# Kernel optimization log

Hardware: AMD Instinct MI355X
Metric: run time of the kernel (lower is better)

Reference implementation:

```python
import jax, jax.numpy as jnp
import numpy as np

B, C, H, W = 2, 1024, 64, 64
R, E, HE, T, K = 16, 4, 512, 3, 2


def setup_inputs() -> dict:
    key = jax.random.key(0)
    ks = jax.random.split(key, 12)
    s = 0.02
    return {
        "x": jax.random.normal(ks[0], (B, C, H, W), jnp.float32),
        "t": jax.random.normal(ks[1], (B, C, H, W), jnp.float32),
        "fc_w": jax.random.normal(ks[2], (C, 2 * C), jnp.float32) * s,
        "ln_g": jnp.ones((C,), jnp.float32),
        "ln_b": jnp.zeros((C,), jnp.float32),
        "f1_w1": jax.random.normal(ks[3], (C // R, C), jnp.float32) * s,
        "f1_b1": jnp.zeros((C // R,), jnp.float32),
        "f1_wa": jax.random.normal(ks[4], (C, C // R), jnp.float32) * s,
        "f1_ba": jnp.zeros((C,), jnp.float32),
        "f1_wb": jax.random.normal(ks[5], (C, C // R), jnp.float32) * s,
        "f1_bb": jnp.zeros((C,), jnp.float32),
        "w_gate": jax.random.normal(ks[6], (T, C, E), jnp.float32) * s,
        "e_w1": jax.random.normal(ks[7], (E, C, HE), jnp.float32) * s,
        "e_b1": jnp.zeros((E, HE), jnp.float32),
        "e_w2": jax.random.normal(ks[8], (E, HE, C), jnp.float32) * s,
        "e_b2": jnp.zeros((E, C), jnp.float32),
        "task_index": 1,
    }


def _cv_squared(v):
    eps = 1e-10
    return jnp.var(v, ddof=1) / (jnp.mean(v) ** 2 + eps)


def reference(x, t, fc_w, ln_g, ln_b, f1_w1, f1_b1, f1_wa, f1_ba, f1_wb, f1_bb,
              w_gate, e_w1, e_b1, e_w2, e_b2, task_index):
    b, c, h, w = x.shape
    n = h * w
    # MultiTaskGeneralFusion: SE-style dual-branch channel gating
    s = jnp.mean(x + t, axis=(2, 3))                        # [B, C]
    hid = jax.nn.relu(s @ f1_w1.T + f1_b1)                  # [B, C/r]
    a = hid @ f1_wa.T + f1_ba                               # [B, C]
    bb = hid @ f1_wb.T + f1_bb                              # [B, C]
    wts = jax.nn.softmax(jnp.stack([a, bb], axis=0), axis=0)  # [2, B, C]
    z = wts[0][:, :, None, None] * x + wts[1][:, :, None, None] * t
    # fused linear -> ReLU -> LayerNorm on concatenated tokens
    x3 = x.reshape(b, c, n).transpose(0, 2, 1)              # [B, N, C]
    t3 = t.reshape(b, c, n).transpose(0, 2, 1)
    y = jnp.concatenate([x3, t3], axis=-1)                  # [B, N, 2C]
    y = jax.nn.relu(jnp.einsum('bnd,cd->bnc', y, fc_w))     # [B, N, C]
    mu = jnp.mean(y, axis=-1, keepdims=True)
    var = jnp.mean((y - mu) ** 2, axis=-1, keepdims=True)
    y = (y - mu) * jax.lax.rsqrt(var + 1e-5) * ln_g + ln_b
    yf = y.reshape(b * n, c)                                # [BN, C]
    # MMoE top-k gating (eval mode: no gating noise)
    logits = yf @ w_gate[task_index]                        # [BN, E]
    top_logits, top_idx = jax.lax.top_k(logits, K)          # [BN, K]
    top_gates = jax.nn.softmax(top_logits, axis=-1)
    gates = jnp.zeros_like(logits).at[jnp.arange(b * n)[:, None], top_idx].set(top_gates)
    # dense expert compute, gated combine
    eh = jax.nn.relu(jnp.einsum('nc,ech->neh', yf, e_w1) + e_b1)   # [BN, E, HE]
    eo = jnp.einsum('neh,eho->neo', eh, e_w2) + e_b2               # [BN, E, C]
    ym = jnp.einsum('ne,neo->no', gates, eo)                        # [BN, C]
    importance = gates.sum(axis=0)
    load = (gates > 0).sum(axis=0).astype(jnp.float32)
    aux_loss = _cv_squared(importance) + _cv_squared(load)
    y4 = ym.reshape(b, n, c).transpose(0, 2, 1).reshape(b, c, h, w) + z
    return (y4, aux_loss)
```

## Files before the change

kernel.cpp:

```cpp
#include <hip/hip_runtime.h>
#include <cstddef>
#include <cstdint>

#define B_   2
#define C_   1024
#define N_   4096
#define M_   8192
#define K2_  2048
#define E_   4
#define HE_  512

typedef float f32x4 __attribute__((ext_vector_type(4)));
typedef short bf16x8 __attribute__((ext_vector_type(8)));
typedef _Float16 f16x8 __attribute__((ext_vector_type(8)));
typedef unsigned short u16x8 __attribute__((ext_vector_type(8)));

#define WAITV(N) asm volatile("s_waitcnt vmcnt(" #N ")" ::: "memory")
#define WAITL0   asm volatile("s_waitcnt lgkmcnt(0)" ::: "memory")
#define SBAR     __builtin_amdgcn_sched_barrier(0)

static __device__ __forceinline__ unsigned short f2bf(float f) {
  unsigned int u = __float_as_uint(f);
  u = u + 0x7fffu + ((u >> 16) & 1u);
  return (unsigned short)(u >> 16);
}

static __device__ __forceinline__ void gl_lds16(const void* g, void* l) {
  __builtin_amdgcn_global_load_lds(
      (const __attribute__((address_space(1))) void*)(uintptr_t)g,
      (__attribute__((address_space(3))) void*)(unsigned)(uintptr_t)l,
      16, 0, 0);
}

__global__ __launch_bounds__(256) void k_se_gate(const float* __restrict__ s,
                                                 const float* __restrict__ w1, const float* __restrict__ b1,
                                                 const float* __restrict__ wa, const float* __restrict__ ba,
                                                 const float* __restrict__ wb, const float* __restrict__ bbv,
                                                 float* __restrict__ wts0) {
  __shared__ float hid[2][64];
  const int t = threadIdx.x;
  if (t < 128) {
    const int b = t >> 6, r = t & 63;
    float acc = b1[r];
    const float* sp = s + b * C_;
    const float* wp = w1 + r * C_;
    for (int c = 0; c < C_; ++c) acc = fmaf(sp[c], wp[c], acc);
    hid[b][r] = fmaxf(acc, 0.f);
  }
  __syncthreads();
  for (int o = t; o < B_ * C_; o += 256) {
    const int b = o >> 10, c = o & 1023;
    float a = ba[c], bb = bbv[c];
    #pragma unroll 8
    for (int r = 0; r < 64; ++r) {
      const float h = hid[b][r];
      a  = fmaf(h, wa[c * 64 + r], a);
      bb = fmaf(h, wb[c * 64 + r], bb);
    }
    wts0[o] = 1.f / (1.f + expf(bb - a));
  }
}

__global__ __launch_bounds__(256) void k_prep_act(const float* __restrict__ x,
                                                  const float* __restrict__ t,
                                                  _Float16* __restrict__ ah,
                                                  _Float16* __restrict__ am,
                                                  float* __restrict__ spart) {
  __shared__ float tile[64][65];
  const int c0 = blockIdx.x * 64, n0 = blockIdx.y * 64, b = blockIdx.z;
  const float* xb = x + (size_t)b * (C_ * N_);
  const float* tb = t + (size_t)b * (C_ * N_);
  _Float16* ahb = ah + (size_t)b * (N_ * (size_t)K2_);
  _Float16* amb = am + (size_t)b * (N_ * (size_t)K2_);
  const int tid = threadIdx.x;
  const int prow = tid >> 2, pseg = tid & 3;
  float psum = 0.f;
  #pragma unroll
  for (int srcsel = 0; srcsel < 2; ++srcsel) {
    const float* src = srcsel ? tb : xb;
    const int koff = srcsel ? C_ : 0;
    if (srcsel) __syncthreads();
    #pragma unroll
    for (int p = 0; p < 4; ++p) {
      const int f = tid + p * 256;
      const int cr = f >> 4, nq = f & 15;
      const float4 v = *(const float4*)(src + (size_t)(c0 + cr) * N_ + n0 + nq * 4);
      tile[cr][nq * 4 + 0] = v.x; tile[cr][nq * 4 + 1] = v.y;
      tile[cr][nq * 4 + 2] = v.z; tile[cr][nq * 4 + 3] = v.w;
    }
    __syncthreads();
    {
      float a = 0.f;
      #pragma unroll
      for (int u = 0; u < 16; ++u) a += tile[prow][pseg * 16 + u];
      psum += a;
    }
    #pragma unroll
    for (int p = 0; p < 2; ++p) {
      const int f = tid + p * 256;
      const int mr = f >> 3, kq = f & 7;
      f16x8 hv, mv;
      #pragma unroll
      for (int u = 0; u < 8; ++u) {
        const float v = tile[kq * 8 + u][mr] * 64.f;
        const _Float16 h = (_Float16)v;
        hv[u] = h;
        mv[u] = (_Float16)(v - (float)h);
      }
      const size_t off = (size_t)(n0 + mr) * K2_ + koff + c0 + kq * 8;
      *(f16x8*)(ahb + off) = hv;
      *(f16x8*)(amb + off) = mv;
    }
  }
  psum += __shfl_xor(psum, 1);
  psum += __shfl_xor(psum, 2);
  if (pseg == 0)
    spart[((size_t)(b * C_ + c0 + prow)) * 64 + blockIdx.y] = psum;
}

__global__ __launch_bounds__(256) void k_reduce2(const float* __restrict__ spart,
                                                 float* __restrict__ s) {
  const int idx = blockIdx.x * 256 + threadIdx.x;
  const float* p = spart + (size_t)idx * 64;
  float acc = 0.f;
  #pragma unroll
  for (int j = 0; j < 64; ++j) acc += p[j];
  s[idx] = acc * (1.f / (float)N_);
}

__global__ __launch_bounds__(256) void k_prep_fcw(const float* __restrict__ w,
                                                  _Float16* __restrict__ wh,
                                                  _Float16* __restrict__ wm) {
  const size_t i = ((size_t)blockIdx.x * 256 + threadIdx.x) * 8;
  const float4 v0 = *(const float4*)(w + i);
  const float4 v1 = *(const float4*)(w + i + 4);
  const float vv[8] = {v0.x, v0.y, v0.z, v0.w, v1.x, v1.y, v1.z, v1.w};
  f16x8 hv, mv;
  #pragma unroll
  for (int u = 0; u < 8; ++u) {
    const float sv = vv[u] * 4096.f;
    const _Float16 h = (_Float16)sv;
    hv[u] = h;
    mv[u] = (_Float16)(sv - (float)h);
  }
  *(f16x8*)(wh + i) = hv;
  *(f16x8*)(wm + i) = mv;
}

__global__ __launch_bounds__(256) void k_prep_tr(const float* __restrict__ src, long long zs, int srs,
                                                 unsigned short* __restrict__ dst, long long zo, int drs) {
  __shared__ float tile[64][65];
  const int c0 = blockIdx.x * 64, r0 = blockIdx.y * 64, z = blockIdx.z;
  const float* s = src + (size_t)z * zs;
  unsigned short* d = dst + (size_t)z * zo;
  const int tid = threadIdx.x;
  #pragma unroll
  for (int p = 0; p < 4; ++p) {
    const int f = tid + p * 256;
    const int rr = f >> 4, cq = f & 15;
    const float4 v = *(const float4*)(s + (size_t)(r0 + rr) * srs + c0 + cq * 4);
    tile[rr][cq * 4 + 0] = v.x; tile[rr][cq * 4 + 1] = v.y;
    tile[rr][cq * 4 + 2] = v.z; tile[rr][cq * 4 + 3] = v.w;
  }
  __syncthreads();
  #pragma unroll
  for (int p = 0; p < 2; ++p) {
    const int f = tid + p * 256;
    const int cr = f >> 3, rq = f & 7;
    u16x8 o;
    #pragma unroll
    for (int u = 0; u < 8; ++u) o[u] = f2bf(tile[rq * 8 + u][cr]);
    *(u16x8*)(d + (size_t)(c0 + cr) * drs + r0 + rq * 8) = o;
  }
}

__global__ __launch_bounds__(256) void k_fc_mfma(const _Float16* __restrict__ Ah,
                                                 const _Float16* __restrict__ Am,
                                                 const _Float16* __restrict__ Bh,
                                                 const _Float16* __restrict__ Bm,
                                                 float* __restrict__ y) {
  __shared__ __align__(16) char lds[2][32768];
  const int tid = threadIdx.x, w = tid >> 6, l = tid & 63;
  const int flat = blockIdx.x + blockIdx.y * 8;
  const int swz = (flat & 7) * 64 + (flat >> 3);
  const int n0 = (swz & 7) * 128, m0 = (swz >> 3) * 128;
  const int wr = w >> 1, wc = w & 1, lg = l >> 4, lr = l & 15;
  f32x4 acc[4][4] = {};
  const int sg = tid >> 7, sr = tid & 127;
  const size_t ga0 = (size_t)(m0 + sr) * K2_ + sg * 8;
  const size_t gb0 = (size_t)(n0 + sr) * K2_ + sg * 8;

  auto STAGE = [&](int buf, int k0) {
    char* b = &lds[buf][0] + w * 1024;
    gl_lds16(Ah + ga0 + k0, b);
    gl_lds16(Ah + ga0 + 16 + k0, b + 4096);
    gl_lds16(Am + ga0 + k0, b + 8192);
    gl_lds16(Am + ga0 + 16 + k0, b + 12288);
    gl_lds16(Bh + gb0 + k0, b + 16384);
    gl_lds16(Bh + gb0 + 16 + k0, b + 20480);
    gl_lds16(Bm + gb0 + k0, b + 24576);
    gl_lds16(Bm + gb0 + 16 + k0, b + 28672);
  };

  STAGE(0, 0);
  STAGE(1, 32);
  for (int it = 0; it < 64; ++it) {
    const int cur = it & 1;
    if (it < 63) { WAITV(8); } else { WAITV(0); }
    SBAR;
    __builtin_amdgcn_s_barrier();
    const char* bb = &lds[cur][0];
    f16x8 a_h[4], a_m[4], b_h[4], b_m[4];
    #pragma unroll
    for (int i = 0; i < 4; ++i) {
      const int off = lg * 2048 + (wr * 64 + i * 16 + lr) * 16;
      a_h[i] = *(const f16x8*)(bb + off);
      a_m[i] = *(const f16x8*)(bb + 8192 + off);
    }
    #pragma unroll
    for (int j = 0; j < 4; ++j) {
      const int off = lg * 2048 + (wc * 64 + j * 16 + lr) * 16;
      b_h[j] = *(const f16x8*)(bb + 16384 + off);
      b_m[j] = *(const f16x8*)(bb + 24576 + off);
    }
    #pragma unroll
    for (int i = 0; i < 4; ++i)
      #pragma unroll
      for (int j = 0; j < 4; ++j)
        acc[i][j] = __builtin_amdgcn_mfma_f32_16x16x32_f16(a_h[i], b_h[j], acc[i][j], 0, 0, 0);
    #pragma unroll
    for (int i = 0; i < 4; ++i)
      #pragma unroll
      for (int j = 0; j < 4; ++j)
        acc[i][j] = __builtin_amdgcn_mfma_f32_16x16x32_f16(a_h[i], b_m[j], acc[i][j], 0, 0, 0);
    #pragma unroll
    for (int i = 0; i < 4; ++i)
      #pragma unroll
      for (int j = 0; j < 4; ++j)
        acc[i][j] = __builtin_amdgcn_mfma_f32_16x16x32_f16(a_m[i], b_h[j], acc[i][j], 0, 0, 0);
    WAITL0;
    SBAR;
    __builtin_amdgcn_s_barrier();
    if (it < 62) STAGE(cur, (it + 2) * 32);
  }
  #pragma unroll
  for (int i = 0; i < 4; ++i) {
    const int mb = m0 + wr * 64 + i * 16 + lg * 4;
    #pragma unroll
    for (int j = 0; j < 4; ++j) {
      const int n = n0 + wc * 64 + j * 16 + lr;
      #pragma unroll
      for (int r = 0; r < 4; ++r)
        y[(size_t)(mb + r) * C_ + n] = fmaxf(acc[i][j][r] * (1.f / 262144.f), 0.f);
    }
  }
}

__global__ __launch_bounds__(256) void k_ln_topk(const float* __restrict__ y,
                                                 const float* __restrict__ lng, const float* __restrict__ lnb,
                                                 const float* __restrict__ wg, const int* __restrict__ taskp,
                                                 unsigned short* __restrict__ yf, float* __restrict__ gates) {
  const int wv = threadIdx.x >> 6, ln = threadIdx.x & 63;
  const int m = blockIdx.x * 4 + wv;
  const float* yr = y + (size_t)m * C_;
  float4 v[4];
  #pragma unroll
  for (int ch = 0; ch < 4; ++ch) v[ch] = *(const float4*)(yr + ch * 256 + ln * 4);
  float sum = 0.f;
  #pragma unroll
  for (int ch = 0; ch < 4; ++ch) sum += (v[ch].x + v[ch].y) + (v[ch].z + v[ch].w);
  #pragma unroll
  for (int o = 32; o; o >>= 1) sum += __shfl_down(sum, o);
  sum = __shfl(sum, 0);
  const float mu = sum * (1.f / 1024.f);
  float q = 0.f;
  #pragma unroll
  for (int ch = 0; ch < 4; ++ch) {
    const float dx = v[ch].x - mu, dy = v[ch].y - mu, dz = v[ch].z - mu, dw = v[ch].w - mu;
    q += (dx * dx + dy * dy) + (dz * dz + dw * dw);
  }
  #pragma unroll
  for (int o = 32; o; o >>= 1) q += __shfl_down(q, o);
  q = __shfl(q, 0);
  const float rstd = rsqrtf(q * (1.f / 1024.f) + 1e-5f);
  const float* wrow = wg + (size_t)(*taskp) * (C_ * E_);
  float l0 = 0.f, l1 = 0.f, l2 = 0.f, l3 = 0.f;
  #pragma unroll
  for (int ch = 0; ch < 4; ++ch) {
    const int c = ch * 256 + ln * 4;
    const float4 gg = *(const float4*)(lng + c);
    const float4 bv = *(const float4*)(lnb + c);
    float f[4];
    f[0] = (v[ch].x - mu) * rstd * gg.x + bv.x;
    f[1] = (v[ch].y - mu) * rstd * gg.y + bv.y;
    f[2] = (v[ch].z - mu) * rstd * gg.z + bv.z;
    f[3] = (v[ch].w - mu) * rstd * gg.w + bv.w;
    uint2 pk;
    pk.x = (unsigned)f2bf(f[0]) | ((unsigned)f2bf(f[1]) << 16);
    pk.y = (unsigned)f2bf(f[2]) | ((unsigned)f2bf(f[3]) << 16);
    *(uint2*)(yf + (size_t)m * C_ + c) = pk;
    #pragma unroll
    for (int i = 0; i < 4; ++i) {
      const float4 we = *(const float4*)(wrow + (size_t)(c + i) * 4);
      l0 = fmaf(f[i], we.x, l0); l1 = fmaf(f[i], we.y, l1);
      l2 = fmaf(f[i], we.z, l2); l3 = fmaf(f[i], we.w, l3);
    }
  }
  #pragma unroll
  for (int o = 32; o; o >>= 1) {
    l0 += __shfl_down(l0, o); l1 += __shfl_down(l1, o);
    l2 += __shfl_down(l2, o); l3 += __shfl_down(l3, o);
  }
  if (ln == 0) {
    const float L[4] = {l0, l1, l2, l3};
    int i1 = 0; float best = L[0];
    #pragma unroll
    for (int e = 1; e < 4; ++e) if (L[e] > best) { best = L[e]; i1 = e; }
    int i2 = -1; float s2 = 0.f;
    #pragma unroll
    for (int e = 0; e < 4; ++e) if (e != i1 && (i2 < 0 || L[e] > s2)) { s2 = L[e]; i2 = e; }
    const float g1 = 1.f / (1.f + expf(s2 - best));
    const float g2 = 1.f - g1;
    float4 gv;
    gv.x = (i1 == 0) ? g1 : ((i2 == 0) ? g2 : 0.f);
    gv.y = (i1 == 1) ? g1 : ((i2 == 1) ? g2 : 0.f);
    gv.z = (i1 == 2) ? g1 : ((i2 == 2) ? g2 : 0.f);
    gv.w = (i1 == 3) ? g1 : ((i2 == 3) ? g2 : 0.f);
    *(float4*)(gates + (size_t)m * 4) = gv;
  }
}

__global__ __launch_bounds__(256) void k_moe1_mfma(const unsigned short* __restrict__ yf,
                                                   const short* __restrict__ Bw,
                                                   const float* __restrict__ b1,
                                                   const float* __restrict__ gates,
                                                   unsigned short* __restrict__ ehg) {
  __shared__ __align__(16) char lds[2][16384];
  const int tid = threadIdx.x, w = tid >> 6, l = tid & 63;
  const int flat = blockIdx.x + blockIdx.y * 16;
  const int swz = (flat & 7) * 128 + (flat >> 3);
  const int n0 = (swz & 15) * 128, m0 = (swz >> 4) * 128;
  const int wr = w >> 1, wc = w & 1, lg = l >> 4, lr = l & 15;
  f32x4 acc[4][4] = {};
  const int sg = tid >> 7, sr = tid & 127;
  const size_t ga0 = (size_t)(m0 + sr) * C_ + sg * 8;
  const size_t gb0 = (size_t)(n0 + sr) * C_ + sg * 8;

  auto STAGE = [&](int buf, int k0) {
    char* b = &lds[buf][0] + w * 1024;
    gl_lds16(yf + ga0 + k0, b);
    gl_lds16(yf + ga0 + 16 + k0, b + 4096);
    gl_lds16(Bw + gb0 + k0, b + 8192);
    gl_lds16(Bw + gb0 + 16 + k0, b + 12288);
  };

  STAGE(0, 0);
  STAGE(1, 32);
  for (int it = 0; it < 32; ++it) {
    const int cur = it & 1;
    if (it < 31) { WAITV(4); } else { WAITV(0); }
    SBAR;
    __builtin_amdgcn_s_barrier();
    const char* bb = &lds[cur][0];
    bf16x8 af[4], bfr[4];
    #pragma unroll
    for (int i = 0; i < 4; ++i)
      af[i] = *(const bf16x8*)(bb + lg * 2048 + (wr * 64 + i * 16 + lr) * 16);
    #pragma unroll
    for (int j = 0; j < 4; ++j)
      bfr[j] = *(const bf16x8*)(bb + 8192 + lg * 2048 + (wc * 64 + j * 16 + lr) * 16);
    SBAR;
    __builtin_amdgcn_s_setprio(1);
    #pragma unroll
    for (int i = 0; i < 4; ++i)
      #pragma unroll
      for (int j = 0; j < 4; ++j)
        acc[i][j] = __builtin_amdgcn_mfma_f32_16x16x32_bf16(af[i], bfr[j], acc[i][j], 0, 0, 0);
    __builtin_amdgcn_s_setprio(0);
    WAITL0;
    SBAR;
    __builtin_amdgcn_s_barrier();
    if (it < 30) STAGE(cur, (it + 2) * 32);
  }
  const int e0 = n0 >> 9;
  #pragma unroll
  for (int j = 0; j < 4; ++j) {
    const int n = n0 + wc * 64 + j * 16 + lr;
    const float bias = b1[e0 * HE_ + (n & 511)];
    #pragma unroll
    for (int i = 0; i < 4; ++i) {
      const int mb = m0 + wr * 64 + i * 16 + lg * 4;
      #pragma unroll
      for (int r = 0; r < 4; ++r) {
        const float g = gates[(size_t)(mb + r) * 4 + e0];
        const float v = fmaxf(acc[i][j][r] + bias, 0.f) * g;
        ehg[(size_t)(mb + r) * K2_ + n] = f2bf(v);
      }
    }
  }
}

__global__ __launch_bounds__(256) void k_moe2_mfma(const short* __restrict__ Aeh,
                                                   const short* __restrict__ Bw,
                                                   const float* __restrict__ b2,
                                                   const float* __restrict__ gates,
                                                   float* __restrict__ ym) {
  __shared__ __align__(16) char lds[2][16384];
  const int tid = threadIdx.x, w = tid >> 6, l = tid & 63;
  const int flat = blockIdx.x + blockIdx.y * 8;
  const int swz = (flat & 7) * 64 + (flat >> 3);
  const int n0 = (swz & 7) * 128, m0 = (swz >> 3) * 128;
  const int wr = w >> 1, wc = w & 1, lg = l >> 4, lr = l & 15;
  f32x4 acc[4][4] = {};
  const int sg = tid >> 7, sr = tid & 127;
  const size_t ga0 = (size_t)(m0 + sr) * K2_ + sg * 8;
  const size_t gb0 = (size_t)(n0 + sr) * K2_ + sg * 8;

  auto STAGE = [&](int buf, int k0) {
    char* b = &lds[buf][0] + w * 1024;
    gl_lds16(Aeh + ga0 + k0, b);
    gl_lds16(Aeh + ga0 + 16 + k0, b + 4096);
    gl_lds16(Bw + gb0 + k0, b + 8192);
    gl_lds16(Bw + gb0 + 16 + k0, b + 12288);
  };

  STAGE(0, 0);
  STAGE(1, 32);
  for (int it = 0; it < 64; ++it) {
    const int cur = it & 1;
    if (it < 63) { WAITV(4); } else { WAITV(0); }
    SBAR;
    __builtin_amdgcn_s_barrier();
    const char* bb = &lds[cur][0];
    bf16x8 af[4], bfr[4];
    #pragma unroll
    for (int i = 0; i < 4; ++i)
      af[i] = *(const bf16x8*)(bb + lg * 2048 + (wr * 64 + i * 16 + lr) * 16);
    #pragma unroll
    for (int j = 0; j < 4; ++j)
      bfr[j] = *(const bf16x8*)(bb + 8192 + lg * 2048 + (wc * 64 + j * 16 + lr) * 16);
    SBAR;
    __builtin_amdgcn_s_setprio(1);
    #pragma unroll
    for (int i = 0; i < 4; ++i)
      #pragma unroll
      for (int j = 0; j < 4; ++j)
        acc[i][j] = __builtin_amdgcn_mfma_f32_16x16x32_bf16(af[i], bfr[j], acc[i][j], 0, 0, 0);
    __builtin_amdgcn_s_setprio(0);
    WAITL0;
    SBAR;
    __builtin_amdgcn_s_barrier();
    if (it < 62) STAGE(cur, (it + 2) * 32);
  }
  float bb2[4][4];
  #pragma unroll
  for (int j = 0; j < 4; ++j) {
    const int n = n0 + wc * 64 + j * 16 + lr;
    #pragma unroll
    for (int e = 0; e < 4; ++e) bb2[j][e] = b2[e * C_ + n];
  }
  #pragma unroll
  for (int i = 0; i < 4; ++i) {
    const int mb = m0 + wr * 64 + i * 16 + lg * 4;
    #pragma unroll
    for (int r = 0; r < 4; ++r) {
      const float4 g = *(const float4*)(gates + (size_t)(mb + r) * 4);
      #pragma unroll
      for (int j = 0; j < 4; ++j) {
        const int n = n0 + wc * 64 + j * 16 + lr;
        ym[(size_t)(mb + r) * C_ + n] =
            acc[i][j][r] + g.x * bb2[j][0] + g.y * bb2[j][1] + g.z * bb2[j][2] + g.w * bb2[j][3];
      }
    }
  }
}

__global__ __launch_bounds__(256) void k_aux(const float* __restrict__ gates, float* __restrict__ outp) {
  const int t = threadIdx.x;
  float imp[4] = {0, 0, 0, 0}, ld[4] = {0, 0, 0, 0};
  for (int m = t; m < M_; m += 256) {
    const float4 g = *(const float4*)(gates + (size_t)m * 4);
    imp[0] += g.x; imp[1] += g.y; imp[2] += g.z; imp[3] += g.w;
    ld[0] += (g.x > 0.f) ? 1.f : 0.f; ld[1] += (g.y > 0.f) ? 1.f : 0.f;
    ld[2] += (g.z > 0.f) ? 1.f : 0.f; ld[3] += (g.w > 0.f) ? 1.f : 0.f;
  }
  __shared__ float red[8][4];
  const int wv = t >> 6, ln = t & 63;
  #pragma unroll
  for (int e = 0; e < 4; ++e) {
    float a = imp[e], b = ld[e];
    #pragma unroll
    for (int o = 32; o; o >>= 1) { a += __shfl_down(a, o); b += __shfl_down(b, o); }
    if (ln == 0) { red[e][wv] = a; red[4 + e][wv] = b; }
  }
  __syncthreads();
  if (t == 0) {
    float I[4], L[4];
    #pragma unroll
    for (int e = 0; e < 4; ++e) {
      I[e] = red[e][0] + red[e][1] + red[e][2] + red[e][3];
      L[e] = red[4 + e][0] + red[4 + e][1] + red[4 + e][2] + red[4 + e][3];
    }
    const float mi = (I[0] + I[1] + I[2] + I[3]) * 0.25f;
    const float vi = ((I[0] - mi) * (I[0] - mi) + (I[1] - mi) * (I[1] - mi) +
                      (I[2] - mi) * (I[2] - mi) + (I[3] - mi) * (I[3] - mi)) / 3.f;
    const float ml = (L[0] + L[1] + L[2] + L[3]) * 0.25f;
    const float vl = ((L[0] - ml) * (L[0] - ml) + (L[1] - ml) * (L[1] - ml) +
                      (L[2] - ml) * (L[2] - ml) + (L[3] - ml) * (L[3] - ml)) / 3.f;
    *outp = vi / (mi * mi + 1e-10f) + vl / (ml * ml + 1e-10f);
  }
}

__global__ __launch_bounds__(256) void k_final(const float* __restrict__ ym,
                                               const float* __restrict__ x, const float* __restrict__ t,
                                               const float* __restrict__ wts0, float* __restrict__ out) {
  __shared__ float tile[64][65];
  const int c0 = blockIdx.x * 64, n0 = blockIdx.y * 64, b = blockIdx.z;
  const int tid = threadIdx.x;
  #pragma unroll
  for (int p = 0; p < 4; ++p) {
    const int f = tid + p * 256;
    const int row = f >> 4, cq = f & 15;
    const float4 v = *(const float4*)(ym + (size_t)(b * N_ + n0 + row) * C_ + c0 + cq * 4);
    tile[row][cq * 4 + 0] = v.x; tile[row][cq * 4 + 1] = v.y;
    tile[row][cq * 4 + 2] = v.z; tile[row][cq * 4 + 3] = v.w;
  }
  __syncthreads();
  #pragma unroll
  for (int p = 0; p < 4; ++p) {
    const int f = tid + p * 256;
    const int cr = f >> 4, nq = f & 15;
    const int c = c0 + cr;
    const float w0 = wts0[b * C_ + c];
    const float w1 = 1.f - w0;
    const size_t idx = (size_t)(b * C_ + c) * N_ + n0 + nq * 4;
    const float4 xv = *(const float4*)(x + idx);
    const float4 tv = *(const float4*)(t + idx);
    float4 o;
    o.x = tile[nq * 4 + 0][cr] + w0 * xv.x + w1 * tv.x;
    o.y = tile[nq * 4 + 1][cr] + w0 * xv.y + w1 * tv.y;
    o.z = tile[nq * 4 + 2][cr] + w0 * xv.z + w1 * tv.z;
    o.w = tile[nq * 4 + 3][cr] + w0 * xv.w + w1 * tv.w;
    *(float4*)(out + idx) = o;
  }
}

extern "C" void kernel_launch(void* const* d_in, const int* in_sizes, int n_in,
                              void* d_out, int out_size, void* d_ws, size_t ws_size,
                              hipStream_t stream) {
  const float* x     = (const float*)d_in[0];
  const float* t     = (const float*)d_in[1];
  const float* fc_w  = (const float*)d_in[2];
  const float* ln_g  = (const float*)d_in[3];
  const float* ln_b  = (const float*)d_in[4];
  const float* f1_w1 = (const float*)d_in[5];
  const float* f1_b1 = (const float*)d_in[6];
  const float* f1_wa = (const float*)d_in[7];
  const float* f1_ba = (const float*)d_in[8];
  const float* f1_wb = (const float*)d_in[9];
  const float* f1_bb = (const float*)d_in[10];
  const float* w_gate = (const float*)d_in[11];
  const float* e_w1  = (const float*)d_in[12];
  const float* e_b1  = (const float*)d_in[13];
  const float* e_w2  = (const float*)d_in[14];
  const float* e_b2  = (const float*)d_in[15];
  const int*   task  = (const int*)d_in[16];
  float* out = (float*)d_out;

  char* ws = (char*)d_ws;
  float*          y     = (float*)ws;
  float*          spart = (float*)ws;
  _Float16*       ah    = (_Float16*)(ws + 33554432);
  _Float16*       am    = (_Float16*)(ws + 67108864);
  unsigned short* yf    = (unsigned short*)(ws + 33554432);
  unsigned short* ehg   = (unsigned short*)(ws + 50331648);
  _Float16* wh  = (_Float16*)(ws + 100663296);
  _Float16* wm  = (_Float16*)(ws + 104857600);
  short*    w1t = (short*)(ws + 109051904);
  short*    w2t = (short*)(ws + 113246208);
  float* sbuf  = (float*)(ws + 117440512);
  float* wts0  = (float*)(ws + 117448704);
  float* gates = (float*)(ws + 117456896);

  k_prep_fcw<<<1024, 256, 0, stream>>>(fc_w, wh, wm);
  k_prep_tr<<<dim3(8, 16, 4), 256, 0, stream>>>(e_w1, 524288LL, 512, (unsigned short*)w1t, 524288LL, 1024);
  k_prep_tr<<<dim3(16, 8, 4), 256, 0, stream>>>(e_w2, 524288LL, 1024, (unsigned short*)w2t, 512LL, 2048);
  k_prep_act<<<dim3(16, 64, 2), 256, 0, stream>>>(x, t, ah, am, spart);
  k_reduce2<<<8, 256, 0, stream>>>(spart, sbuf);
  k_se_gate<<<1, 256, 0, stream>>>(sbuf, f1_w1, f1_b1, f1_wa, f1_ba, f1_wb, f1_bb, wts0);
  k_fc_mfma<<<dim3(8, 64), 256, 0, stream>>>(ah, am, wh, wm, y);
  k_ln_topk<<<M_ / 4, 256, 0, stream>>>(y, ln_g, ln_b, w_gate, task, yf, gates);
  k_moe1_mfma<<<dim3(16, 64), 256, 0, stream>>>(yf, w1t, e_b1, gates, ehg);
  k_moe2_mfma<<<dim3(8, 64), 256, 0, stream>>>((const short*)ehg, w2t, e_b2, gates, y);
  k_aux<<<1, 256, 0, stream>>>(gates, out + (size_t)B_ * C_ * N_);
  k_final<<<dim3(C_ / 64, N_ / 64, B_), 256, 0, stream>>>(y, x, t, wts0, out);
}
```

Measured before the change: 416.6 us.

## Enlarge FC GEMM tile to 256x128 with 512 threads and phased prefetch

The fused-linear GEMM kernel moves from 256-thread 128x128 tiles to 512-thread 256x128 tiles, so each B tile is reused across more rows. The global-to-LDS prefetch of the next K slice is split into three phases, each placed between the three MFMA groups (hi*hi, hi*lo, lo*hi), with partial vmcnt waits and s_setprio raised around MFMA bursts. The aim is to overlap loads with compute and halve B traffic. In exchange it uses more LDS (96KB per block), more barriers per iteration, and launches half as many blocks.

```diff
diff --git a/kernel.cpp b/kernel.cpp
--- a/kernel.cpp
+++ b/kernel.cpp
@@ -174,74 +174,125 @@
   }
 }
 
-__global__ __launch_bounds__(256) void k_fc_mfma(const _Float16* __restrict__ Ah,
-                                                 const _Float16* __restrict__ Am,
-                                                 const _Float16* __restrict__ Bh,
-                                                 const _Float16* __restrict__ Bm,
-                                                 float* __restrict__ y) {
-  __shared__ __align__(16) char lds[2][32768];
+__global__ __launch_bounds__(512, 2) void k_fc_mfma(const _Float16* __restrict__ Ah,
+                                                    const _Float16* __restrict__ Am,
+                                                    const _Float16* __restrict__ Bh,
+                                                    const _Float16* __restrict__ Bm,
+                                                    float* __restrict__ y) {
+  __shared__ __align__(16) char lds[2][49152];
   const int tid = threadIdx.x, w = tid >> 6, l = tid & 63;
   const int flat = blockIdx.x + blockIdx.y * 8;
-  const int swz = (flat & 7) * 64 + (flat >> 3);
-  const int n0 = (swz & 7) * 128, m0 = (swz >> 3) * 128;
+  const int swz = (flat & 7) * 32 + (flat >> 3);
+  const int n0 = (swz & 7) * 128, m0 = (swz >> 3) * 256;
   const int wr = w >> 1, wc = w & 1, lg = l >> 4, lr = l & 15;
   f32x4 acc[4][4] = {};
-  const int sg = tid >> 7, sr = tid & 127;
-  const size_t ga0 = (size_t)(m0 + sr) * K2_ + sg * 8;
-  const size_t gb0 = (size_t)(n0 + sr) * K2_ + sg * 8;
-
-  auto STAGE = [&](int buf, int k0) {
-    char* b = &lds[buf][0] + w * 1024;
-    gl_lds16(Ah + ga0 + k0, b);
-    gl_lds16(Ah + ga0 + 16 + k0, b + 4096);
-    gl_lds16(Am + ga0 + k0, b + 8192);
-    gl_lds16(Am + ga0 + 16 + k0, b + 12288);
-    gl_lds16(Bh + gb0 + k0, b + 16384);
-    gl_lds16(Bh + gb0 + 16 + k0, b + 20480);
-    gl_lds16(Bm + gb0 + k0, b + 24576);
-    gl_lds16(Bm + gb0 + 16 + k0, b + 28672);
+
+  auto LDA = [&](char* bufb, const _Float16* src, int roff, int k0, int q) {
+    const int chunk = q * 512 + tid;
+    const int kg = chunk >> 8, row = chunk & 255;
+    gl_lds16(src + (size_t)(m0 + row) * K2_ + k0 + kg * 8,
+             bufb + roff + (q * 512 + w * 64) * 16);
   };
-
-  STAGE(0, 0);
-  STAGE(1, 32);
-  for (int it = 0; it < 64; ++it) {
-    const int cur = it & 1;
-    if (it < 63) { WAITV(8); } else { WAITV(0); }
-    SBAR;
-    __builtin_amdgcn_s_barrier();
+  auto LDB = [&](char* bufb, const _Float16* src, int roff, int k0) {
+    const int kg = tid >> 7, row = tid & 127;
+    gl_lds16(src + (size_t)(n0 + row) * K2_ + k0 + kg * 8,
+             bufb + roff + (w * 64) * 16);
+  };
+
+  LDA(&lds[0][0], Ah, 0, 0, 0);
+  LDA(&lds[0][0], Ah, 0, 0, 1);
+  LDB(&lds[0][0], Bh, 32768, 0);
+  LDB(&lds[0][0], Bm, 40960, 0);
+  LDA(&lds[0][0], Am, 16384, 0, 0);
+  LDA(&lds[0][0], Am, 16384, 0, 1);
+
+  f16x8 a_h[4], b_h[4], b_m[4], a_m[4];
+  for (int t = 0; t < 63; ++t) {
+    const int cur = t & 1;
     const char* bb = &lds[cur][0];
-    f16x8 a_h[4], a_m[4], b_h[4], b_m[4];
-    #pragma unroll
-    for (int i = 0; i < 4; ++i) {
-      const int off = lg * 2048 + (wr * 64 + i * 16 + lr) * 16;
-      a_h[i] = *(const f16x8*)(bb + off);
-      a_m[i] = *(const f16x8*)(bb + 8192 + off);
-    }
-    #pragma unroll
-    for (int j = 0; j < 4; ++j) {
-      const int off = lg * 2048 + (wc * 64 + j * 16 + lr) * 16;
-      b_h[j] = *(const f16x8*)(bb + 16384 + off);
-      b_m[j] = *(const f16x8*)(bb + 24576 + off);
-    }
+    char* nb = &lds[cur ^ 1][0];
+    const int nk = (t + 1) * 32;
+    WAITV(3); SBAR;
+    __builtin_amdgcn_s_barrier();
+    LDA(nb, Ah, 0, nk, 0);
+    LDA(nb, Ah, 0, nk, 1);
+    #pragma unroll
+    for (int i = 0; i < 4; ++i)
+      a_h[i] = *(const f16x8*)(bb + (lg * 256 + wr * 64 + i * 16 + lr) * 16);
+    #pragma unroll
+    for (int j = 0; j < 4; ++j)
+      b_h[j] = *(const f16x8*)(bb + 32768 + (lg * 128 + wc * 64 + j * 16 + lr) * 16);
+    __builtin_amdgcn_s_setprio(1);
     #pragma unroll
     for (int i = 0; i < 4; ++i)
       #pragma unroll
       for (int j = 0; j < 4; ++j)
         acc[i][j] = __builtin_amdgcn_mfma_f32_16x16x32_f16(a_h[i], b_h[j], acc[i][j], 0, 0, 0);
+    __builtin_amdgcn_s_setprio(0);
+    WAITV(4); SBAR;
+    __builtin_amdgcn_s_barrier();
+    LDB(nb, Bh, 32768, nk);
+    LDB(nb, Bm, 40960, nk);
+    #pragma unroll
+    for (int j = 0; j < 4; ++j)
+      b_m[j] = *(const f16x8*)(bb + 40960 + (lg * 128 + wc * 64 + j * 16 + lr) * 16);
+    __builtin_amdgcn_s_setprio(1);
     #pragma unroll
     for (int i = 0; i < 4; ++i)
       #pragma unroll
       for (int j = 0; j < 4; ++j)
         acc[i][j] = __builtin_amdgcn_mfma_f32_16x16x32_f16(a_h[i], b_m[j], acc[i][j], 0, 0, 0);
+    __builtin_amdgcn_s_setprio(0);
+    WAITV(4); SBAR;
+    __builtin_amdgcn_s_barrier();
+    LDA(nb, Am, 16384, nk, 0);
+    LDA(nb, Am, 16384, nk, 1);
+    #pragma unroll
+    for (int i = 0; i < 4; ++i)
+      a_m[i] = *(const f16x8*)(bb + 16384 + (lg * 256 + wr * 64 + i * 16 + lr) * 16);
+    __builtin_amdgcn_s_setprio(1);
     #pragma unroll
     for (int i = 0; i < 4; ++i)
       #pragma unroll
       for (int j = 0; j < 4; ++j)
         acc[i][j] = __builtin_amdgcn_mfma_f32_16x16x32_f16(a_m[i], b_h[j], acc[i][j], 0, 0, 0);
-    WAITL0;
-    SBAR;
-    __builtin_amdgcn_s_barrier();
-    if (it < 62) STAGE(cur, (it + 2) * 32);
+    __builtin_amdgcn_s_setprio(0);
+  }
+  {
+    const char* bb = &lds[1][0];
+    WAITV(3); SBAR;
+    __builtin_amdgcn_s_barrier();
+    #pragma unroll
+    for (int i = 0; i < 4; ++i)
+      a_h[i] = *(const f16x8*)(bb + (lg * 256 + wr * 64 + i * 16 + lr) * 16);
+    #pragma unroll
+    for (int j = 0; j < 4; ++j)
+      b_h[j] = *(const f16x8*)(bb + 32768 + (lg * 128 + wc * 64 + j * 16 + lr) * 16);
+    #pragma unroll
+    for (int i = 0; i < 4; ++i)
+      #pragma unroll
+      for (int j = 0; j < 4; ++j)
+        acc[i][j] = __builtin_amdgcn_mfma_f32_16x16x32_f16(a_h[i], b_h[j], acc[i][j], 0, 0, 0);
+    WAITV(2); SBAR;
+    __builtin_amdgcn_s_barrier();
+    #pragma unroll
+    for (int j = 0; j < 4; ++j)
+      b_m[j] = *(const f16x8*)(bb + 40960 + (lg * 128 + wc * 64 + j * 16 + lr) * 16);
+    #pragma unroll
+    for (int i = 0; i < 4; ++i)
+      #pragma unroll
+      for (int j = 0; j < 4; ++j)
+        acc[i][j] = __builtin_amdgcn_mfma_f32_16x16x32_f16(a_h[i], b_m[j], acc[i][j], 0, 0, 0);
+    WAITV(0); SBAR;
+    __builtin_amdgcn_s_barrier();
+    #pragma unroll
+    for (int i = 0; i < 4; ++i)
+      a_m[i] = *(const f16x8*)(bb + 16384 + (lg * 256 + wr * 64 + i * 16 + lr) * 16);
+    #pragma unroll
+    for (int i = 0; i < 4; ++i)
+      #pragma unroll
+      for (int j = 0; j < 4; ++j)
+        acc[i][j] = __builtin_amdgcn_mfma_f32_16x16x32_f16(a_m[i], b_h[j], acc[i][j], 0, 0, 0);
   }
   #pragma unroll
   for (int i = 0; i < 4; ++i) {
@@ -588,7 +639,7 @@
   k_prep_act<<<dim3(16, 64, 2), 256, 0, stream>>>(x, t, ah, am, spart);
   k_reduce2<<<8, 256, 0, stream>>>(spart, sbuf);
   k_se_gate<<<1, 256, 0, stream>>>(sbuf, f1_w1, f1_b1, f1_wa, f1_ba, f1_wb, f1_bb, wts0);
-  k_fc_mfma<<<dim3(8, 64), 256, 0, stream>>>(ah, am, wh, wm, y);
+  k_fc_mfma<<<dim3(8, 32), 512, 0, stream>>>(ah, am, wh, wm, y);
   k_ln_topk<<<M_ / 4, 256, 0, stream>>>(y, ln_g, ln_b, w_gate, task, yf, gates);
   k_moe1_mfma<<<dim3(16, 64), 256, 0, stream>>>(yf, w1t, e_b1, gates, ehg);
   k_moe2_mfma<<<dim3(8, 64), 256, 0, stream>>>((const short*)ehg, w2t, e_b2, gates, y);
```

Result: faster. 407.0 us (-2.3%).

## Triple-buffer LDS in GEMM kernels and enlarge fc tile to 256x128

Applied to the files above, without the earlier changes.

The three MFMA GEMM kernels move from double to triple LDS buffering. The next stage's global-to-LDS loads are now issued right after the single per-iteration barrier, which removes the second barrier and the lgkmcnt wait. k_fc_mfma also grows to 512 threads with a 256x128 output tile, so each B tile is shared by twice as many rows, and it raises MFMA priority with setprio. The cost is more LDS per block (147KB for fc), which may limit occupancy and depends on the three-stage WAR reasoning being correct.

```diff
diff --git a/kernel.cpp b/kernel.cpp
--- a/kernel.cpp
+++ b/kernel.cpp
@@ -16,7 +16,6 @@
 typedef unsigned short u16x8 __attribute__((ext_vector_type(8)));
 
 #define WAITV(N) asm volatile("s_waitcnt vmcnt(" #N ")" ::: "memory")
-#define WAITL0   asm volatile("s_waitcnt lgkmcnt(0)" ::: "memory")
 #define SBAR     __builtin_amdgcn_sched_barrier(0)
 
 static __device__ __forceinline__ unsigned short f2bf(float f) {
@@ -174,55 +173,63 @@
   }
 }
 
-__global__ __launch_bounds__(256) void k_fc_mfma(const _Float16* __restrict__ Ah,
-                                                 const _Float16* __restrict__ Am,
-                                                 const _Float16* __restrict__ Bh,
-                                                 const _Float16* __restrict__ Bm,
-                                                 float* __restrict__ y) {
-  __shared__ __align__(16) char lds[2][32768];
+__global__ __launch_bounds__(512, 2) void k_fc_mfma(const _Float16* __restrict__ Ah,
+                                                    const _Float16* __restrict__ Am,
+                                                    const _Float16* __restrict__ Bh,
+                                                    const _Float16* __restrict__ Bm,
+                                                    float* __restrict__ y) {
+  __shared__ __align__(16) char lds[3][49152];
   const int tid = threadIdx.x, w = tid >> 6, l = tid & 63;
   const int flat = blockIdx.x + blockIdx.y * 8;
-  const int swz = (flat & 7) * 64 + (flat >> 3);
-  const int n0 = (swz & 7) * 128, m0 = (swz >> 3) * 128;
+  const int swz = (flat & 7) * 32 + (flat >> 3);
+  const int n0 = (swz & 7) * 128, m0 = (swz >> 3) * 256;
   const int wr = w >> 1, wc = w & 1, lg = l >> 4, lr = l & 15;
   f32x4 acc[4][4] = {};
-  const int sg = tid >> 7, sr = tid & 127;
-  const size_t ga0 = (size_t)(m0 + sr) * K2_ + sg * 8;
-  const size_t gb0 = (size_t)(n0 + sr) * K2_ + sg * 8;
-
+
+  auto LDA = [&](char* bufb, const _Float16* src, int roff, int k0, int q) {
+    const int chunk = q * 512 + tid;
+    const int kg = chunk >> 8, row = chunk & 255;
+    gl_lds16(src + (size_t)(m0 + row) * K2_ + k0 + kg * 8,
+             bufb + roff + (q * 512 + w * 64) * 16);
+  };
+  auto LDB = [&](char* bufb, const _Float16* src, int roff, int k0) {
+    const int kg = tid >> 7, row = tid & 127;
+    gl_lds16(src + (size_t)(n0 + row) * K2_ + k0 + kg * 8,
+             bufb + roff + (w * 64) * 16);
+  };
   auto STAGE = [&](int buf, int k0) {
-    char* b = &lds[buf][0] + w * 1024;
-    gl_lds16(Ah + ga0 + k0, b);
-    gl_lds16(Ah + ga0 + 16 + k0, b + 4096);
-    gl_lds16(Am + ga0 + k0, b + 8192);
-    gl_lds16(Am + ga0 + 16 + k0, b + 12288);
-    gl_lds16(Bh + gb0 + k0, b + 16384);
-    gl_lds16(Bh + gb0 + 16 + k0, b + 20480);
-    gl_lds16(Bm + gb0 + k0, b + 24576);
-    gl_lds16(Bm + gb0 + 16 + k0, b + 28672);
+    char* b = &lds[buf][0];
+    LDA(b, Ah, 0, k0, 0);
+    LDA(b, Ah, 0, k0, 1);
+    LDB(b, Bh, 32768, k0);
+    LDB(b, Bm, 40960, k0);
+    LDA(b, Am, 16384, k0, 0);
+    LDA(b, Am, 16384, k0, 1);
   };
 
   STAGE(0, 0);
   STAGE(1, 32);
-  for (int it = 0; it < 64; ++it) {
-    const int cur = it & 1;
-    if (it < 63) { WAITV(8); } else { WAITV(0); }
+  for (int t = 0; t < 64; ++t) {
+    const int cur = t % 3;
+    if (t < 63) { WAITV(6); } else { WAITV(0); }
     SBAR;
     __builtin_amdgcn_s_barrier();
+    if (t < 62) STAGE((t + 2) % 3, (t + 2) * 32);
     const char* bb = &lds[cur][0];
     f16x8 a_h[4], a_m[4], b_h[4], b_m[4];
     #pragma unroll
     for (int i = 0; i < 4; ++i) {
-      const int off = lg * 2048 + (wr * 64 + i * 16 + lr) * 16;
+      const int off = (lg * 256 + wr * 64 + i * 16 + lr) * 16;
       a_h[i] = *(const f16x8*)(bb + off);
-      a_m[i] = *(const f16x8*)(bb + 8192 + off);
+      a_m[i] = *(const f16x8*)(bb + 16384 + off);
     }
     #pragma unroll
     for (int j = 0; j < 4; ++j) {
-      const int off = lg * 2048 + (wc * 64 + j * 16 + lr) * 16;
-      b_h[j] = *(const f16x8*)(bb + 16384 + off);
-      b_m[j] = *(const f16x8*)(bb + 24576 + off);
-    }
+      const int off = (lg * 128 + wc * 64 + j * 16 + lr) * 16;
+      b_h[j] = *(const f16x8*)(bb + 32768 + off);
+      b_m[j] = *(const f16x8*)(bb + 40960 + off);
+    }
+    __builtin_amdgcn_s_setprio(1);
     #pragma unroll
     for (int i = 0; i < 4; ++i)
       #pragma unroll
@@ -238,10 +245,7 @@
       #pragma unroll
       for (int j = 0; j < 4; ++j)
         acc[i][j] = __builtin_amdgcn_mfma_f32_16x16x32_f16(a_m[i], b_h[j], acc[i][j], 0, 0, 0);
-    WAITL0;
-    SBAR;
-    __builtin_amdgcn_s_barrier();
-    if (it < 62) STAGE(cur, (it + 2) * 32);
+    __builtin_amdgcn_s_setprio(0);
   }
   #pragma unroll
   for (int i = 0; i < 4; ++i) {
@@ -335,7 +339,7 @@
                                                    const float* __restrict__ b1,
                                                    const float* __restrict__ gates,
                                                    unsigned short* __restrict__ ehg) {
-  __shared__ __align__(16) char lds[2][16384];
+  __shared__ __align__(16) char lds[3][16384];
   const int tid = threadIdx.x, w = tid >> 6, l = tid & 63;
   const int flat = blockIdx.x + blockIdx.y * 16;
   const int swz = (flat & 7) * 128 + (flat >> 3);
@@ -357,10 +361,11 @@
   STAGE(0, 0);
   STAGE(1, 32);
   for (int it = 0; it < 32; ++it) {
-    const int cur = it & 1;
+    const int cur = it % 3;
     if (it < 31) { WAITV(4); } else { WAITV(0); }
     SBAR;
     __builtin_amdgcn_s_barrier();
+    if (it < 30) STAGE((it + 2) % 3, (it + 2) * 32);
     const char* bb = &lds[cur][0];
     bf16x8 af[4], bfr[4];
     #pragma unroll
@@ -369,7 +374,6 @@
     #pragma unroll
     for (int j = 0; j < 4; ++j)
       bfr[j] = *(const bf16x8*)(bb + 8192 + lg * 2048 + (wc * 64 + j * 16 + lr) * 16);
-    SBAR;
     __builtin_amdgcn_s_setprio(1);
     #pragma unroll
     for (int i = 0; i < 4; ++i)
@@ -377,10 +381,6 @@
       for (int j = 0; j < 4; ++j)
         acc[i][j] = __builtin_amdgcn_mfma_f32_16x16x32_bf16(af[i], bfr[j], acc[i][j], 0, 0, 0);
     __builtin_amdgcn_s_setprio(0);
-    WAITL0;
-    SBAR;
-    __builtin_amdgcn_s_barrier();
-    if (it < 30) STAGE(cur, (it + 2) * 32);
   }
   const int e0 = n0 >> 9;
   #pragma unroll
@@ -405,7 +405,7 @@
                                                    const float* __restrict__ b2,
                                                    const float* __restrict__ gates,
                                                    float* __restrict__ ym) {
-  __shared__ __align__(16) char lds[2][16384];
+  __shared__ __align__(16) char lds[3][16384];
   const int tid = threadIdx.x, w = tid >> 6, l = tid & 63;
   const int flat = blockIdx.x + blockIdx.y * 8;
   const int swz = (flat & 7) * 64 + (flat >> 3);
@@ -427,10 +427,11 @@
   STAGE(0, 0);
   STAGE(1, 32);
   for (int it = 0; it < 64; ++it) {
-    const int cur = it & 1;
+    const int cur = it % 3;
     if (it < 63) { WAITV(4); } else { WAITV(0); }
     SBAR;
     __builtin_amdgcn_s_barrier();
+    if (it < 62) STAGE((it + 2) % 3, (it + 2) * 32);
     const char* bb = &lds[cur][0];
     bf16x8 af[4], bfr[4];
     #pragma unroll
@@ -439,7 +440,6 @@
     #pragma unroll
     for (int j = 0; j < 4; ++j)
       bfr[j] = *(const bf16x8*)(bb + 8192 + lg * 2048 + (wc * 64 + j * 16 + lr) * 16);
-    SBAR;
     __builtin_amdgcn_s_setprio(1);
     #pragma unroll
     for (int i = 0; i < 4; ++i)
@@ -447,10 +447,6 @@
       for (int j = 0; j < 4; ++j)
         acc[i][j] = __builtin_amdgcn_mfma_f32_16x16x32_bf16(af[i], bfr[j], acc[i][j], 0, 0, 0);
     __builtin_amdgcn_s_setprio(0);
-    WAITL0;
-    SBAR;
-    __builtin_amdgcn_s_barrier();
-    if (it < 62) STAGE(cur, (it + 2) * 32);
   }
   float bb2[4][4];
   #pragma unroll
@@ -588,7 +584,7 @@
   k_prep_act<<<dim3(16, 64, 2), 256, 0, stream>>>(x, t, ah, am, spart);
   k_reduce2<<<8, 256, 0, stream>>>(spart, sbuf);
   k_se_gate<<<1, 256, 0, stream>>>(sbuf, f1_w1, f1_b1, f1_wa, f1_ba, f1_wb, f1_bb, wts0);
-  k_fc_mfma<<<dim3(8, 64), 256, 0, stream>>>(ah, am, wh, wm, y);
+  k_fc_mfma<<<dim3(8, 32), 512, 0, stream>>>(ah, am, wh, wm, y);
   k_ln_topk<<<M_ / 4, 256, 0, stream>>>(y, ln_g, ln_b, w_gate, task, yf, gates);
   k_moe1_mfma<<<dim3(16, 64), 256, 0, stream>>>(yf, w1t, e_b1, gates, ehg);
   k_moe2_mfma<<<dim3(8, 64), 256, 0, stream>>>((const short*)ehg, w2t, e_b2, gates, y);
```

After: 423.1 us. About the same (+1.6%).
